# Performance work log

Hardware: AMD Instinct MI355X
Metric: run time of the kernel (lower is better)

Reference implementation:

```python
import jax, jax.numpy as jnp
import numpy as np

ALPHA = 4.0  # spikingjelly sigmoid surrogate alpha
EPS = 1e-5   # BatchNorm eps
TAU = 2.0
NUM_HEADS = 8

@jax.custom_vjp
def _spike(x):
    return (x >= 0.0).astype(x.dtype)

def _spike_fwd(x):
    return _spike(x), x

def _spike_bwd(x, g):
    s = jax.nn.sigmoid(ALPHA * x)
    return (g * ALPHA * s * (1.0 - s),)

_spike.defvjp(_spike_fwd, _spike_bwd)

def lif(x, v_th=1.0):
    # MultiStepLIFNode: v += (x - v)/tau, spike = H(v - v_th), hard reset to 0 (detached)
    def step(v, xt):
        v = v + (xt - v) / TAU
        s = _spike(v - v_th)
        v = v * (1.0 - jax.lax.stop_gradient(s))
        return v, s
    _, spikes = jax.lax.scan(step, jnp.zeros_like(x[0]), x)
    return spikes

def bn(x, gamma, beta, mean, var):
    sh = (1, 1, -1, 1, 1)  # channel axis 2 of [T,B,C,H,W]
    inv = gamma.reshape(sh) / jnp.sqrt(var.reshape(sh) + EPS)
    return (x - mean.reshape(sh)) * inv + beta.reshape(sh)

def setup_inputs() -> dict:
    T, B, C, H, W = 4, 16, 384, 32, 32
    key = jax.random.key(0)
    ks = jax.random.split(key, 10)
    def wmat(k):
        return jax.random.normal(k, (C, C), jnp.float32) * 0.05
    def bn_params(k):
        k1, k2, k3, k4 = jax.random.split(k, 4)
        return (jax.random.uniform(k1, (C,), jnp.float32, 0.5, 1.5),
                jax.random.normal(k2, (C,), jnp.float32) * 0.1,
                jax.random.normal(k3, (C,), jnp.float32) * 0.1,
                jax.random.uniform(k4, (C,), jnp.float32, 0.5, 1.5))
    qg, qb, qm, qv = bn_params(ks[2])
    kg, kb, km, kv_ = bn_params(ks[3])
    vg, vb, vm, vv = bn_params(ks[4])
    pg, pb, pm, pv = bn_params(ks[5])
    return {
        'x': jax.random.normal(ks[0], (T, B, C, H, W), jnp.float32),
        'q_w': wmat(ks[1]), 'q_gamma': qg, 'q_beta': qb, 'q_mean': qm, 'q_var': qv,
        'k_w': wmat(ks[6]), 'k_gamma': kg, 'k_beta': kb, 'k_mean': km, 'k_var': kv_,
        'v_w': wmat(ks[7]), 'v_gamma': vg, 'v_beta': vb, 'v_mean': vm, 'v_var': vv,
        'proj_w': wmat(ks[8]), 'proj_b': jax.random.normal(ks[9], (C,), jnp.float32) * 0.02,
        'proj_gamma': pg, 'proj_beta': pb, 'proj_mean': pm, 'proj_var': pv,
    }

def reference(x, q_w, q_gamma, q_beta, q_mean, q_var,
              k_w, k_gamma, k_beta, k_mean, k_var,
              v_w, v_gamma, v_beta, v_mean, v_var,
              proj_w, proj_b, proj_gamma, proj_beta, proj_mean, proj_var):
    T, B, C, H, W = x.shape
    N = H * W
    h = NUM_HEADS
    d = C // h
    identity = x
    xs = lif(x)  # shortcut_lif

    def branch(w_, g_, b_, m_, var_):
        y = jnp.einsum('tbchw,dc->tbdhw', xs, w_)  # conv1x1, no bias
        return lif(bn(y, g_, b_, m_, var_))

    def to_heads(t):  # [T,B,C,H,W] -> [T,B,h,N,d]
        return (t.reshape(T, B, C, N).transpose(0, 1, 3, 2)
                 .reshape(T, B, N, h, d).transpose(0, 1, 3, 2, 4))

    q = to_heads(branch(q_w, q_gamma, q_beta, q_mean, q_var))
    k = to_heads(branch(k_w, k_gamma, k_beta, k_mean, k_var))
    v = to_heads(branch(v_w, v_gamma, v_beta, v_mean, v_var))

    kv = lif((k * v).sum(axis=3, keepdims=True), v_th=0.5)  # [T,B,h,1,d]
    out = q * kv  # [T,B,h,N,d]
    out = out.transpose(0, 1, 2, 4, 3).reshape(T, B, C, H, W)
    out = jnp.einsum('tbchw,dc->tbdhw', out, proj_w) + proj_b.reshape(1, 1, -1, 1, 1)
    out = bn(out, proj_gamma, proj_beta, proj_mean, proj_var)
    return (out + identity, v)
```

## Files before the change

### kernel.cpp

```cpp
#include <hip/hip_runtime.h>
#include <math.h>

#define T_ 4
#define B_ 16
#define C_ 384
#define N_ 1024
#define CN_ (C_ * N_)
#define BCN_ (B_ * CN_)
#define TBCN_ (T_ * BCN_)
#define HEADS_ 8
#define DH_ 48
#define EPS_ 1e-5f
#define NW_ 12
#define M3_ 1152

typedef float f4 __attribute__((ext_vector_type(4)));
typedef float f2 __attribute__((ext_vector_type(2)));


__global__ __launch_bounds__(256) void prep_wt_qkv(
        const float* __restrict__ qw, const float* __restrict__ kw,
        const float* __restrict__ vw, float* __restrict__ Wt) {
    int idx = blockIdx.x * 256 + threadIdx.x;
    int m = idx / C_, c = idx % C_;
    Wt[(size_t)c * M3_ + m]       = qw[idx];
    Wt[(size_t)c * M3_ + 384 + m] = kw[idx];
    Wt[(size_t)c * M3_ + 768 + m] = vw[idx];
}

__global__ __launch_bounds__(256) void prep_wt_proj(
        const float* __restrict__ pw, float* __restrict__ Wtp) {
    int idx = blockIdx.x * 256 + threadIdx.x;
    int r = idx / C_, m = idx % C_;
    int Wb = r >> 5, i = r & 31;
    int c = (Wb < 8) ? (128 * (Wb & 1) + 4 * i + (Wb >> 1))
                     : (256 + 4 * i + (Wb - 8));
    Wtp[(size_t)r * C_ + m] = pw[(size_t)m * C_ + c];
}

__global__ __launch_bounds__(256) void prep_bn(
        const float* __restrict__ qg, const float* __restrict__ qb,
        const float* __restrict__ qm, const float* __restrict__ qv,
        const float* __restrict__ kg, const float* __restrict__ kb,
        const float* __restrict__ km, const float* __restrict__ kv2,
        const float* __restrict__ vg, const float* __restrict__ vb,
        const float* __restrict__ vm, const float* __restrict__ vv,
        float* __restrict__ invA, float* __restrict__ muA, float* __restrict__ beA) {
    int i = blockIdx.x * 256 + threadIdx.x;
    if (i >= M3_) return;
    int br = i / C_, c = i % C_;
    const float *g, *bb, *mm, *va;
    if (br == 0)      { g = qg; bb = qb; mm = qm; va = qv; }
    else if (br == 1) { g = kg; bb = kb; mm = km; va = kv2; }
    else              { g = vg; bb = vb; mm = vm; va = vv; }
    invA[i] = g[c] / sqrtf(va[c] + EPS_);
    muA[i]  = mm[c];
    beA[i]  = bb[c];
}

__global__ __launch_bounds__(256) void lif_x_mask(const float* __restrict__ x,
                                                  unsigned* __restrict__ mask_x) {
    int n  = blockIdx.x * 256 + threadIdx.x;
    int cw = blockIdx.y;
    int b  = blockIdx.z;
    unsigned wrd[T_] = {0u, 0u, 0u, 0u};
    const float* xb = x + (size_t)b * CN_ + (size_t)cw * 32 * N_ + n;
#pragma unroll 4
    for (int cb = 0; cb < 32; ++cb) {
        const float* xp = xb + (size_t)cb * N_;
        float v = 0.f;
#pragma unroll
        for (int t = 0; t < T_; ++t) {
            float xt = xp[(size_t)t * BCN_];
            v = v + (xt - v) * 0.5f;
            if (v >= 1.0f) { wrd[t] |= (1u << cb); v = 0.f; }
        }
    }
#pragma unroll
    for (int t = 0; t < T_; ++t)
        mask_x[((size_t)(t * B_ + b) * NW_ + cw) * N_ + n] = wrd[t];
}

__global__ __launch_bounds__(256) void qkv_sparse(
        const unsigned* __restrict__ mask_x, const float* __restrict__ Wt,
        const float* __restrict__ invA, const float* __restrict__ muA,
        const float* __restrict__ beA,
        unsigned* __restrict__ mq, unsigned* __restrict__ mk,
        unsigned* __restrict__ mv) {
    const int lane = threadIdx.x & 63;
    const int col  = threadIdx.x >> 6;
    const int n = blockIdx.x * 4 + col;
    const int b = blockIdx.y;

    f4 vs[4] = {f4{0.f,0.f,0.f,0.f}, f4{0.f,0.f,0.f,0.f},
                f4{0.f,0.f,0.f,0.f}, f4{0.f,0.f,0.f,0.f}};
    f2 vs4 = f2{0.f, 0.f};

    for (int t = 0; t < T_; ++t) {
        const size_t base = (size_t)(t * B_ + b) * NW_ * N_ + n;
        const unsigned* mp = mask_x + base;
        unsigned bwv[NW_];
#pragma unroll
        for (int w = 0; w < NW_; ++w) bwv[w] = mp[(size_t)w * N_];

        f4 acc[4] = {f4{0.f,0.f,0.f,0.f}, f4{0.f,0.f,0.f,0.f},
                     f4{0.f,0.f,0.f,0.f}, f4{0.f,0.f,0.f,0.f}};
        f2 acc4 = f2{0.f, 0.f};

        for (int w = 0; w < NW_; ++w) {
            unsigned bits = __builtin_amdgcn_readfirstlane(bwv[w]);
            const float* wb0 = Wt + (size_t)(w * 32) * M3_;
            while (bits) {
                int cb0 = __builtin_ctz(bits); bits &= bits - 1;
                const float* r0 = wb0 + (size_t)cb0 * M3_;
                f4 d00 = *(const f4*)(r0 + 4 * lane);
                f4 d01 = *(const f4*)(r0 + 256 + 4 * lane);
                f4 d02 = *(const f4*)(r0 + 512 + 4 * lane);
                f4 d03 = *(const f4*)(r0 + 768 + 4 * lane);
                f2 d04 = *(const f2*)(r0 + 1024 + 2 * lane);
                if (bits) {
                    int cb1 = __builtin_ctz(bits); bits &= bits - 1;
                    const float* r1 = wb0 + (size_t)cb1 * M3_;
                    f4 d10 = *(const f4*)(r1 + 4 * lane);
                    f4 d11 = *(const f4*)(r1 + 256 + 4 * lane);
                    f4 d12 = *(const f4*)(r1 + 512 + 4 * lane);
                    f4 d13 = *(const f4*)(r1 + 768 + 4 * lane);
                    f2 d14 = *(const f2*)(r1 + 1024 + 2 * lane);
                    acc[0] += d00; acc[1] += d01; acc[2] += d02; acc[3] += d03;
                    acc4 += d04;
                    acc[0] += d10; acc[1] += d11; acc[2] += d12; acc[3] += d13;
                    acc4 += d14;
                } else {
                    acc[0] += d00; acc[1] += d01; acc[2] += d02; acc[3] += d03;
                    acc4 += d04;
                }
            }
        }

        unsigned* dq = mq + base;
        unsigned* dk = mk + base;
        unsigned* dv = mv + base;
#pragma unroll
        for (int g = 0; g < 4; ++g) {
            f4 iv = *(const f4*)(invA + g * 256 + 4 * lane);
            f4 mu = *(const f4*)(muA + g * 256 + 4 * lane);
            f4 be = *(const f4*)(beA + g * 256 + 4 * lane);
            f4 pre = (acc[g] - mu) * iv + be;
            f4 v2 = vs[g] + (pre - vs[g]) * 0.5f;
#pragma unroll
            for (int q = 0; q < 4; ++q) {
                bool s = (v2[q] >= 1.0f);
                vs[g][q] = s ? 0.f : v2[q];
                unsigned long long bal = __ballot(s);
                if (lane == 0) {
                    unsigned lo = (unsigned)bal, hi = (unsigned)(bal >> 32);
                    if (g == 0) {
                        dq[(size_t)(2 * q) * N_] = lo;
                        dq[(size_t)(2 * q + 1) * N_] = hi;
                    } else if (g == 1) {
                        dq[(size_t)(8 + q) * N_] = lo;
                        dk[(size_t)q * N_] = hi;
                    } else if (g == 2) {
                        dk[(size_t)(4 + 2 * q) * N_] = lo;
                        dk[(size_t)(5 + 2 * q) * N_] = hi;
                    } else {
                        dv[(size_t)(2 * q) * N_] = lo;
                        dv[(size_t)(2 * q + 1) * N_] = hi;
                    }
                }
            }
        }
        {
            f2 iv = *(const f2*)(invA + 1024 + 2 * lane);
            f2 mu = *(const f2*)(muA + 1024 + 2 * lane);
            f2 be = *(const f2*)(beA + 1024 + 2 * lane);
            f2 pre = (acc4 - mu) * iv + be;
            f2 v2 = vs4 + (pre - vs4) * 0.5f;
#pragma unroll
            for (int q = 0; q < 2; ++q) {
                bool s = (v2[q] >= 1.0f);
                vs4[q] = s ? 0.f : v2[q];
                unsigned long long bal = __ballot(s);
                if (lane == 0) {
                    dv[(size_t)(8 + 2 * q) * N_] = (unsigned)bal;
                    dv[(size_t)(9 + 2 * q) * N_] = (unsigned)(bal >> 32);
                }
            }
        }
    }
}

__global__ __launch_bounds__(384) void kv_count(const unsigned* __restrict__ mk,
                                                const unsigned* __restrict__ mv,
                                                int* __restrict__ cnt) {
    int tb = blockIdx.x;
    int w = threadIdx.x >> 5, chunk = threadIdx.x & 31;
    __shared__ int sc[C_];
    if (threadIdx.x < C_) sc[threadIdx.x] = 0;
    __syncthreads();
    const unsigned* kp = mk + ((size_t)tb * NW_ + w) * N_ + chunk * 32;
    const unsigned* vp = mv + ((size_t)tb * NW_ + w) * N_ + chunk * 32;
    int loc[32];
#pragma unroll
    for (int bit = 0; bit < 32; ++bit) loc[bit] = 0;
#pragma unroll
    for (int i = 0; i < 32; ++i) {
        unsigned a = kp[i] & vp[i];
#pragma unroll
        for (int bit = 0; bit < 32; ++bit) loc[bit] += (int)((a >> bit) & 1u);
    }
#pragma unroll
    for (int bit = 0; bit < 32; ++bit)
        if (loc[bit]) atomicAdd(&sc[w * 32 + bit], loc[bit]);
    __syncthreads();
    if (threadIdx.x < C_) cnt[(size_t)tb * C_ + threadIdx.x] = sc[threadIdx.x];
}

__global__ __launch_bounds__(384) void kv_lif(const int* __restrict__ cnt,
                                              unsigned* __restrict__ kvw) {
    int b = blockIdx.x, c = threadIdx.x;
    float u = 0.f;
    for (int t = 0; t < T_; ++t) {
        float ct = (float)cnt[(size_t)(t * B_ + b) * C_ + c];
        u = u + (ct - u) * 0.5f;
        bool s = (u >= 0.5f);
        u = s ? 0.f : u;
        unsigned long long bal = __ballot(s);
        if ((c & 63) == 0) {
            int wv = c >> 6;
            kvw[(size_t)(t * B_ + b) * NW_ + wv * 2]     = (unsigned)bal;
            kvw[(size_t)(t * B_ + b) * NW_ + wv * 2 + 1] = (unsigned)(bal >> 32);
        }
    }
}

__global__ __launch_bounds__(256) void v_to_out1(const unsigned* __restrict__ mv,
                                                 float* __restrict__ out1) {
    int tb = blockIdx.y;
    int n0 = blockIdx.x * 128;
    __shared__ unsigned ws_[NW_][128];
    for (int i = threadIdx.x; i < NW_ * 128; i += 256) {
        int w = i >> 7, nn = i & 127;
        ws_[w][nn] = mv[((size_t)tb * NW_ + w) * N_ + n0 + nn];
    }
    __syncthreads();
    float* dst = out1 + (size_t)tb * HEADS_ * N_ * DH_;
    for (int h = 0; h < HEADS_; ++h) {
        float* dh = dst + ((size_t)h * N_ + n0) * DH_;
#pragma unroll
        for (int l = 0; l < 24; ++l) {
            int flat = l * 256 + threadIdx.x;
            int nn = flat / DH_, dd = flat - nn * DH_;
            int c = h * DH_ + dd;
            int Wb, bit;
            if (c < 256) { Wb = 2 * (c & 3) + (c >> 7); bit = (c & 127) >> 2; }
            else { int r = c - 256; Wb = 8 + 2 * (r & 1) + (r >> 6); bit = (r & 63) >> 1; }
            unsigned wd = ws_[Wb][nn];
            dh[flat] = (float)((wd >> bit) & 1u);
        }
    }
}

__global__ __launch_bounds__(256) void proj_out0(
        const unsigned* __restrict__ mq, const unsigned* __restrict__ kvw,
        const float* __restrict__ Wtp, const float* __restrict__ pb,
        const float* __restrict__ pg, const float* __restrict__ pbe,
        const float* __restrict__ pm, const float* __restrict__ pv,
        const float* __restrict__ x, float* __restrict__ out0) {
    int tb = blockIdx.y;
    int n0 = blockIdx.x * 64;
    int m0 = blockIdx.z * 128;
    __shared__ float acc[128][65];
    const int lane = threadIdx.x & 63, wv = threadIdx.x >> 6;

    unsigned kvr[NW_];
    const unsigned* kvp = kvw + (size_t)tb * NW_;
#pragma unroll
    for (int w = 0; w < NW_; ++w) kvr[w] = kvp[w];

    for (int ci = 0; ci < 16; ++ci) {
        int coln = wv * 16 + ci;
        const unsigned* mp = mq + (size_t)tb * NW_ * N_ + n0 + coln;
        unsigned bw[NW_];
#pragma unroll
        for (int w = 0; w < NW_; ++w) bw[w] = mp[(size_t)w * N_] & kvr[w];

        float a0 = 0.f, a1 = 0.f, b0 = 0.f, b1 = 0.f;
#pragma unroll
        for (int w = 0; w < NW_; ++w) {
            unsigned bits = bw[w];
            while (bits) {
                int cb0 = __builtin_ctz(bits);
                bits &= bits - 1;
                const float* wr0 = Wtp + (size_t)(w * 32 + cb0) * C_ + m0 + lane;
                if (bits) {
                    int cb1 = __builtin_ctz(bits);
                    bits &= bits - 1;
                    const float* wr1 = Wtp + (size_t)(w * 32 + cb1) * C_ + m0 + lane;
                    float x00 = wr0[0], x01 = wr0[64];
                    float x10 = wr1[0], x11 = wr1[64];
                    a0 += x00; a1 += x01;
                    b0 += x10; b1 += x11;
                } else {
                    a0 += wr0[0];
                    a1 += wr0[64];
                }
            }
        }
        acc[lane][coln]      = a0 + b0;
        acc[lane + 64][coln] = a1 + b1;
    }
    __syncthreads();

    const float* xb = x + (size_t)tb * CN_ + (size_t)m0 * N_ + n0;
    float* ob = out0 + (size_t)tb * CN_ + (size_t)m0 * N_ + n0;
    for (int mi = 0; mi < 32; ++mi) {
        int ml = mi * 4 + wv;
        int m = m0 + ml;
        float inv = pg[m] / sqrtf(pv[m] + EPS_);
        float cst = (pb[m] - pm[m]) * inv + pbe[m];
        float a = acc[ml][lane];
        ob[(size_t)ml * N_ + lane] = a * inv + cst + xb[(size_t)ml * N_ + lane];
    }
}

extern "C" void kernel_launch(void* const* d_in, const int* in_sizes, int n_in,
                              void* d_out, int out_size, void* d_ws, size_t ws_size,
                              hipStream_t stream) {
    (void)in_sizes; (void)n_in; (void)out_size; (void)ws_size;
    const float* x      = (const float*)d_in[0];
    const float* q_w    = (const float*)d_in[1];
    const float* q_g    = (const float*)d_in[2];
    const float* q_b    = (const float*)d_in[3];
    const float* q_m    = (const float*)d_in[4];
    const float* q_v    = (const float*)d_in[5];
    const float* k_w    = (const float*)d_in[6];
    const float* k_g    = (const float*)d_in[7];
    const float* k_b    = (const float*)d_in[8];
    const float* k_m    = (const float*)d_in[9];
    const float* k_v    = (const float*)d_in[10];
    const float* v_w    = (const float*)d_in[11];
    const float* v_g    = (const float*)d_in[12];
    const float* v_b    = (const float*)d_in[13];
    const float* v_m    = (const float*)d_in[14];
    const float* v_v    = (const float*)d_in[15];
    const float* proj_w = (const float*)d_in[16];
    const float* proj_b = (const float*)d_in[17];
    const float* p_g    = (const float*)d_in[18];
    const float* p_be   = (const float*)d_in[19];
    const float* p_m    = (const float*)d_in[20];
    const float* p_v    = (const float*)d_in[21];

    float* out0 = (float*)d_out;
    float* out1 = out0 + TBCN_;

    char* p = (char*)d_ws;
    float* Wt_qkv  = (float*)p;    p += (size_t)C_ * M3_ * 4;
    float* Wt_proj = (float*)p;    p += (size_t)C_ * C_ * 4;
    float* invA    = (float*)p;    p += M3_ * 4;
    float* muA     = (float*)p;    p += M3_ * 4;
    float* beA     = (float*)p;    p += M3_ * 4;
    unsigned* mask_x = (unsigned*)p; p += (size_t)T_ * B_ * NW_ * N_ * 4;
    unsigned* mask_q = (unsigned*)p; p += (size_t)T_ * B_ * NW_ * N_ * 4;
    unsigned* mask_k = (unsigned*)p; p += (size_t)T_ * B_ * NW_ * N_ * 4;
    unsigned* mask_v = (unsigned*)p; p += (size_t)T_ * B_ * NW_ * N_ * 4;
    int* cnt       = (int*)p;      p += (size_t)T_ * B_ * C_ * 4;
    unsigned* kvw  = (unsigned*)p; p += (size_t)T_ * B_ * NW_ * 4;

    prep_wt_qkv<<<(C_ * C_) / 256, 256, 0, stream>>>(q_w, k_w, v_w, Wt_qkv);
    prep_wt_proj<<<(C_ * C_) / 256, 256, 0, stream>>>(proj_w, Wt_proj);
    prep_bn<<<(M3_ + 255) / 256, 256, 0, stream>>>(q_g, q_b, q_m, q_v,
                                                   k_g, k_b, k_m, k_v,
                                                   v_g, v_b, v_m, v_v,
                                                   invA, muA, beA);

    lif_x_mask<<<dim3(N_ / 256, NW_, B_), 256, 0, stream>>>(x, mask_x);

    qkv_sparse<<<dim3(N_ / 4, B_), 256, 0, stream>>>(mask_x, Wt_qkv,
                                                     invA, muA, beA,
                                                     mask_q, mask_k, mask_v);

    kv_count<<<T_ * B_, 384, 0, stream>>>(mask_k, mask_v, cnt);
    kv_lif<<<B_, 384, 0, stream>>>(cnt, kvw);

    v_to_out1<<<dim3(N_ / 128, T_ * B_), 256, 0, stream>>>(mask_v, out1);

    proj_out0<<<dim3(N_ / 64, T_ * B_, 3), 256, 0, stream>>>(
        mask_q, kvw, Wt_proj, proj_b, p_g, p_be, p_m, p_v, x, out0);
}
```

Baseline: 569.1 us.

## Precompute active-channel index lists for sparse projection and vectorize out1 stores

```diff
diff --git a/kernel.cpp b/kernel.cpp
--- a/kernel.cpp
+++ b/kernel.cpp
@@ -246,22 +246,104 @@
     __syncthreads();
     float* dst = out1 + (size_t)tb * HEADS_ * N_ * DH_;
     for (int h = 0; h < HEADS_; ++h) {
-        float* dh = dst + ((size_t)h * N_ + n0) * DH_;
-#pragma unroll
-        for (int l = 0; l < 24; ++l) {
-            int flat = l * 256 + threadIdx.x;
-            int nn = flat / DH_, dd = flat - nn * DH_;
-            int c = h * DH_ + dd;
-            int Wb, bit;
-            if (c < 256) { Wb = 2 * (c & 3) + (c >> 7); bit = (c & 127) >> 2; }
-            else { int r = c - 256; Wb = 8 + 2 * (r & 1) + (r >> 6); bit = (r & 63) >> 1; }
-            unsigned wd = ws_[Wb][nn];
-            dh[flat] = (float)((wd >> bit) & 1u);
-        }
-    }
+        f4* dh4 = (f4*)(dst + ((size_t)h * N_ + n0) * DH_);
+#pragma unroll
+        for (int l = 0; l < 6; ++l) {
+            int f4id = l * 256 + threadIdx.x;
+            int nn = f4id / 12, dq = f4id - nn * 12;
+            int dd0 = dq * 4;
+            f4 o;
+#pragma unroll
+            for (int j = 0; j < 4; ++j) {
+                int c = h * DH_ + dd0 + j;
+                int Wb, bit;
+                if (c < 256) { Wb = 2 * (c & 3) + (c >> 7); bit = (c & 127) >> 2; }
+                else { int r = c - 256; Wb = 8 + 2 * (r & 1) + (r >> 6); bit = (r & 63) >> 1; }
+                o[j] = (float)((ws_[Wb][nn] >> bit) & 1u);
+            }
+            dh4[f4id] = o;
+        }
+    }
+}
+
+__global__ __launch_bounds__(256) void build_qlist(
+        const unsigned* __restrict__ mq, const unsigned* __restrict__ kvw,
+        unsigned char* __restrict__ qlist, int* __restrict__ qcnt) {
+    int n = blockIdx.x * 256 + threadIdx.x;
+    int tb = blockIdx.y;
+    const unsigned* mp = mq + (size_t)tb * NW_ * N_ + n;
+    const unsigned* kvp = kvw + (size_t)tb * NW_;
+    unsigned char* dst = qlist + ((size_t)tb * N_ + n) * C_;
+    int cnt = 0;
+    for (int w = 0; w < NW_; ++w) {
+        unsigned bits = mp[(size_t)w * N_] & kvp[w];
+        int base = w * 32;
+        while (bits) {
+            int cb = __builtin_ctz(bits);
+            bits &= bits - 1;
+            dst[cnt++] = (unsigned char)(base + cb);
+        }
+    }
+    qcnt[(size_t)tb * N_ + n] = cnt;
 }
 
 __global__ __launch_bounds__(256) void proj_out0(
+        const unsigned char* __restrict__ qlist, const int* __restrict__ qcnt,
+        const float* __restrict__ Wtp, const float* __restrict__ pb,
+        const float* __restrict__ pg, const float* __restrict__ pbe,
+        const float* __restrict__ pm, const float* __restrict__ pv,
+        const float* __restrict__ x, float* __restrict__ out0) {
+    int tb = blockIdx.y;
+    int n0 = blockIdx.x * 64;
+    int m0 = blockIdx.z * 128;
+    __shared__ float acc[128][65];
+    const int lane = threadIdx.x & 63, wv = threadIdx.x >> 6;
+
+    for (int ci = 0; ci < 16; ++ci) {
+        int coln = wv * 16 + ci;
+        int col = n0 + coln;
+        int cnt = qcnt[(size_t)tb * N_ + col];
+        const unsigned char* lst = qlist + ((size_t)tb * N_ + col) * C_;
+        const float* Wb = Wtp + m0 + lane;
+
+        float a0 = 0.f, a1 = 0.f, b0 = 0.f, b1 = 0.f;
+        float c0 = 0.f, c1 = 0.f, d0 = 0.f, d1 = 0.f;
+        int i = 0;
+        for (; i + 4 <= cnt; i += 4) {
+            unsigned pk = *(const unsigned*)(lst + i);
+            const float* w0 = Wb + (size_t)(pk & 255u) * C_;
+            const float* w1 = Wb + (size_t)((pk >> 8) & 255u) * C_;
+            const float* w2 = Wb + (size_t)((pk >> 16) & 255u) * C_;
+            const float* w3 = Wb + (size_t)(pk >> 24) * C_;
+            float x00 = w0[0], x01 = w0[64];
+            float x10 = w1[0], x11 = w1[64];
+            float x20 = w2[0], x21 = w2[64];
+            float x30 = w3[0], x31 = w3[64];
+            a0 += x00; a1 += x01; b0 += x10; b1 += x11;
+            c0 += x20; c1 += x21; d0 += x30; d1 += x31;
+        }
+        for (; i < cnt; ++i) {
+            const float* w0 = Wb + (size_t)lst[i] * C_;
+            a0 += w0[0]; a1 += w0[64];
+        }
+        acc[lane][coln]      = (a0 + b0) + (c0 + d0);
+        acc[lane + 64][coln] = (a1 + b1) + (c1 + d1);
+    }
+    __syncthreads();
+
+    const float* xb = x + (size_t)tb * CN_ + (size_t)m0 * N_ + n0;
+    float* ob = out0 + (size_t)tb * CN_ + (size_t)m0 * N_ + n0;
+    for (int mi = 0; mi < 32; ++mi) {
+        int ml = mi * 4 + wv;
+        int m = m0 + ml;
+        float inv = pg[m] / sqrtf(pv[m] + EPS_);
+        float cst = (pb[m] - pm[m]) * inv + pbe[m];
+        float a = acc[ml][lane];
+        ob[(size_t)ml * N_ + lane] = a * inv + cst + xb[(size_t)ml * N_ + lane];
+    }
+}
+
+__global__ __launch_bounds__(256) void proj_out0_bits(
         const unsigned* __restrict__ mq, const unsigned* __restrict__ kvw,
         const float* __restrict__ Wtp, const float* __restrict__ pb,
         const float* __restrict__ pg, const float* __restrict__ pbe,
@@ -327,7 +409,7 @@
 extern "C" void kernel_launch(void* const* d_in, const int* in_sizes, int n_in,
                               void* d_out, int out_size, void* d_ws, size_t ws_size,
                               hipStream_t stream) {
-    (void)in_sizes; (void)n_in; (void)out_size; (void)ws_size;
+    (void)in_sizes; (void)n_in; (void)out_size;
     const float* x      = (const float*)d_in[0];
     const float* q_w    = (const float*)d_in[1];
     const float* q_g    = (const float*)d_in[2];
@@ -366,6 +448,11 @@
     unsigned* mask_v = (unsigned*)p; p += (size_t)T_ * B_ * NW_ * N_ * 4;
     int* cnt       = (int*)p;      p += (size_t)T_ * B_ * C_ * 4;
     unsigned* kvw  = (unsigned*)p; p += (size_t)T_ * B_ * NW_ * 4;
+    int* qcnt      = (int*)p;      p += (size_t)T_ * B_ * N_ * 4;
+    unsigned char* qlist = (unsigned char*)p;
+    p += (size_t)T_ * B_ * N_ * C_;
+    const int use_list = (ws_size == 0) ? 0
+                         : (ws_size >= (size_t)(p - (char*)d_ws) ? 1 : 0);
 
     prep_wt_qkv<<<(C_ * C_) / 256, 256, 0, stream>>>(q_w, k_w, v_w, Wt_qkv);
     prep_wt_proj<<<(C_ * C_) / 256, 256, 0, stream>>>(proj_w, Wt_proj);
@@ -385,6 +472,13 @@
 
     v_to_out1<<<dim3(N_ / 128, T_ * B_), 256, 0, stream>>>(mask_v, out1);
 
-    proj_out0<<<dim3(N_ / 64, T_ * B_, 3), 256, 0, stream>>>(
-        mask_q, kvw, Wt_proj, proj_b, p_g, p_be, p_m, p_v, x, out0);
-}
+    if (use_list) {
+        build_qlist<<<dim3(N_ / 256, T_ * B_), 256, 0, stream>>>(mask_q, kvw,
+                                                                 qlist, qcnt);
+        proj_out0<<<dim3(N_ / 64, T_ * B_, 3), 256, 0, stream>>>(
+            qlist, qcnt, Wt_proj, proj_b, p_g, p_be, p_m, p_v, x, out0);
+    } else {
+        proj_out0_bits<<<dim3(N_ / 64, T_ * B_, 3), 256, 0, stream>>>(
+            mask_q, kvw, Wt_proj, proj_b, p_g, p_be, p_m, p_v, x, out0);
+    }
+}
```

After: 560.5 us. No clear change (-1.5%).
